# Performance work log

Measured on AMD Instinct MI355X. Metric: run time of the kernel, lower is better.

Reference implementation:

```python
import jax, jax.numpy as jnp
import numpy as np

N0, N1, F, H1, H2 = 50000, 20000, 128, 64, 32
E00, E01, E10, E11 = 1600000, 1000000, 640000, 640000
K11 = 3  # number of drug-drug relation types


def spmm(rows, cols, vals, X, n_out):
    # sparse (COO) adjacency @ dense X : out[r] += vals[e] * X[cols[e]]
    return jax.ops.segment_sum(vals[:, None] * X[cols], rows, num_segments=n_out)


def setup_inputs() -> dict:
    key = jax.random.key(0)
    ks = jax.random.split(key, 24)
    ri = jax.random.randint
    return {
        'feat0': jax.random.normal(ks[0], (N0, F), jnp.float32),
        'feat1': jax.random.normal(ks[1], (N1, F), jnp.float32),
        'e00_row': ri(ks[2], (E00,), 0, N0, jnp.int32),
        'e00_col': ri(ks[3], (E00,), 0, N0, jnp.int32),
        'e00_val': jax.random.uniform(ks[4], (E00,), jnp.float32),
        'e01_row': ri(ks[5], (E01,), 0, N0, jnp.int32),
        'e01_col': ri(ks[6], (E01,), 0, N1, jnp.int32),
        'e01_val': jax.random.uniform(ks[7], (E01,), jnp.float32),
        'e10_row': ri(ks[8], (E10,), 0, N1, jnp.int32),
        'e10_col': ri(ks[9], (E10,), 0, N0, jnp.int32),
        'e10_val': jax.random.uniform(ks[10], (E10,), jnp.float32),
        'e11_row': ri(ks[11], (K11, E11), 0, N1, jnp.int32),
        'e11_col': ri(ks[12], (K11, E11), 0, N1, jnp.int32),
        'e11_val': jax.random.uniform(ks[13], (K11, E11), jnp.float32),
        'W1_00': jax.random.normal(ks[14], (F, H1), jnp.float32) * 0.05,
        'W1_01': jax.random.normal(ks[15], (F, H1), jnp.float32) * 0.05,
        'W1_10': jax.random.normal(ks[16], (F, H1), jnp.float32) * 0.05,
        'W1_11': jax.random.normal(ks[17], (K11, F, H1), jnp.float32) * 0.05,
        'W2_00': jax.random.normal(ks[18], (H1, H2), jnp.float32) * 0.05,
        'W2_01': jax.random.normal(ks[19], (H1, H2), jnp.float32) * 0.05,
        'W2_10': jax.random.normal(ks[20], (H1, H2), jnp.float32) * 0.05,
        'W2_11': jax.random.normal(ks[21], (K11, H1, H2), jnp.float32) * 0.05,
    }


def reference(feat0, feat1,
              e00_row, e00_col, e00_val,
              e01_row, e01_col, e01_val,
              e10_row, e10_col, e10_val,
              e11_row, e11_col, e11_val,
              W1_00, W1_01, W1_10, W1_11,
              W2_00, W2_01, W2_10, W2_11):
    n0, n1 = feat0.shape[0], feat1.shape[0]

    def multi_spmm(rows_k, cols_k, vals_k, X, W_k, n_out):
        # sum_k adj_k @ (X @ W_k), vmapped over relation types k
        out_k = jax.vmap(lambda r, c, v, W: spmm(r, c, v, X @ W, n_out))(
            rows_k, cols_k, vals_k, W_k)
        return out_k.sum(axis=0)

    # layer 1: GraphConvolutionSparseMulti per edge type, add_n per target type, relu
    h0 = jax.nn.relu(spmm(e00_row, e00_col, e00_val, feat0 @ W1_00, n0)
                     + spmm(e01_row, e01_col, e01_val, feat1 @ W1_01, n0))
    h1 = jax.nn.relu(spmm(e10_row, e10_col, e10_val, feat0 @ W1_10, n1)
                     + multi_spmm(e11_row, e11_col, e11_val, feat1, W1_11, n1))

    # layer 2: GraphConvolutionMulti, add_n per target type (identity act)
    z0 = (spmm(e00_row, e00_col, e00_val, h0 @ W2_00, n0)
          + spmm(e01_row, e01_col, e01_val, h1 @ W2_01, n0))
    z1 = (spmm(e10_row, e10_col, e10_val, h0 @ W2_10, n1)
          + multi_spmm(e11_row, e11_col, e11_val, h1, W2_11, n1))

    # node-type embeddings, concatenated along the node axis: [n0+n1, H2]
    return jnp.concatenate([z0, z1], axis=0)
```

## Files before the change

kernel.cpp:

```cpp
#include <hip/hip_runtime.h>
#include <hip/hip_bf16.h>

constexpr int F = 128, H1 = 64, H2 = 32, K11 = 3;
constexpr int BSH = 6;
constexpr int PARTE = 2048;

static __device__ __forceinline__ float bf_lo(unsigned u) { return __uint_as_float(u << 16); }
static __device__ __forceinline__ float bf_hi(unsigned u) { return __uint_as_float(u & 0xffff0000u); }
static __device__ __forceinline__ unsigned bf16_1(float a) {
    unsigned ua = __float_as_uint(a);
    return (ua + 0x7fffu + ((ua >> 16) & 1u)) >> 16;
}
static __device__ __forceinline__ unsigned pack_bf16(float a, float b) {
    unsigned ua = __float_as_uint(a), ub = __float_as_uint(b);
    unsigned ra = (ua + 0x7fffu + ((ua >> 16) & 1u)) >> 16;
    unsigned rb = (ub + 0x7fffu + ((ub >> 16) & 1u)) & 0xffff0000u;
    return ra | rb;
}

struct GemmB { const float* W[4]; long long cOff[4]; };

template<int FF, int HH, bool ABF16>
__launch_bounds__(256)
__global__ void gemm_b_kernel(const void* __restrict__ Av, GemmB gb,
                              ushort* __restrict__ Cb, int M) {
    const float* __restrict__ W = gb.W[blockIdx.y];
    ushort* C = Cb + gb.cOff[blockIdx.y];
    __shared__ float Ws[FF * HH];
    const int tid = threadIdx.x;
    for (int i = tid * 4; i < FF * HH; i += 1024)
        *reinterpret_cast<float4*>(&Ws[i]) = *reinterpret_cast<const float4*>(&W[i]);
    __syncthreads();

    constexpr int TPR = 4;
    constexpr int CPT = HH / TPR;
    const int t = blockIdx.x * 256 + tid;
    const int row = t / TPR;
    const int sub = t % TPR;
    if (row >= M) return;

    float acc[CPT];
#pragma unroll
    for (int j = 0; j < CPT; ++j) acc[j] = 0.f;

    for (int k = 0; k < FF; k += 8) {
        float av[8];
        if (ABF16) {
            const uint4 u = *reinterpret_cast<const uint4*>((const ushort*)Av + (size_t)row * FF + k);
            av[0] = bf_lo(u.x); av[1] = bf_hi(u.x);
            av[2] = bf_lo(u.y); av[3] = bf_hi(u.y);
            av[4] = bf_lo(u.z); av[5] = bf_hi(u.z);
            av[6] = bf_lo(u.w); av[7] = bf_hi(u.w);
        } else {
            const float* A = (const float*)Av + (size_t)row * FF + k;
            const float4 u0 = *reinterpret_cast<const float4*>(A);
            const float4 u1 = *reinterpret_cast<const float4*>(A + 4);
            av[0] = u0.x; av[1] = u0.y; av[2] = u0.z; av[3] = u0.w;
            av[4] = u1.x; av[5] = u1.y; av[6] = u1.z; av[7] = u1.w;
        }
#pragma unroll
        for (int kk = 0; kk < 8; ++kk) {
            const float* wr = &Ws[(k + kk) * HH + sub * CPT];
#pragma unroll
            for (int j = 0; j < CPT; j += 4) {
                const float4 wv = *reinterpret_cast<const float4*>(&wr[j]);
                acc[j + 0] = fmaf(av[kk], wv.x, acc[j + 0]);
                acc[j + 1] = fmaf(av[kk], wv.y, acc[j + 1]);
                acc[j + 2] = fmaf(av[kk], wv.z, acc[j + 2]);
                acc[j + 3] = fmaf(av[kk], wv.w, acc[j + 3]);
            }
        }
    }
    unsigned packed[CPT / 2];
#pragma unroll
    for (int j = 0; j < CPT; j += 2) packed[j / 2] = pack_bf16(acc[j], acc[j + 1]);
    unsigned* c = (unsigned*)(C + (size_t)row * HH + sub * CPT);
#pragma unroll
    for (int j = 0; j < CPT / 2; j += 4)
        *reinterpret_cast<uint4*>(&c[j]) = make_uint4(packed[j], packed[j + 1], packed[j + 2], packed[j + 3]);
}

struct BinDesc { const int* rows[6]; int E[6]; int n[6]; int binBase[6]; };

__launch_bounds__(256)
__global__ void binhist_kernel(BinDesc d, int* __restrict__ binCnt) {
    const int a = blockIdx.y;
    const int E = d.E[a];
    const int start = blockIdx.x * 8192;
    if (start >= E) return;
    const int nb = (d.n[a] + 63) >> BSH;
    __shared__ int h[1024];
    for (int i = threadIdx.x; i < nb; i += 256) h[i] = 0;
    __syncthreads();
    const int* rows = d.rows[a];
    const int end = min(E, start + 8192);
    for (int e = start + (int)threadIdx.x; e < end; e += 256)
        atomicAdd(&h[rows[e] >> BSH], 1);
    __syncthreads();
    int* bc = binCnt + d.binBase[a];
    for (int i = threadIdx.x; i < nb; i += 256)
        if (h[i]) atomicAdd(&bc[i], h[i]);
}

__launch_bounds__(256)
__global__ void binscan_kernel(const int* __restrict__ binCnt, int* __restrict__ binPtr,
                               int* __restrict__ binCur, int TB, int Etot,
                               int* __restrict__ gptr, int Lidx) {
    __shared__ int lds[256];
    __shared__ int carry;
    if (threadIdx.x == 0) carry = 0;
    __syncthreads();
    for (int base = 0; base < TB; base += 256) {
        const int i = base + threadIdx.x;
        const int v = (i < TB) ? binCnt[i] : 0;
        lds[threadIdx.x] = v;
        __syncthreads();
        for (int o = 1; o < 256; o <<= 1) {
            int t = (threadIdx.x >= o) ? lds[threadIdx.x - o] : 0;
            __syncthreads();
            lds[threadIdx.x] += t;
            __syncthreads();
        }
        const int c = carry;
        __syncthreads();
        if (i < TB) {
            const int excl = c + lds[threadIdx.x] - v;
            binPtr[i] = excl;
            binCur[i] = excl;
        }
        if (threadIdx.x == 255) carry = c + lds[255];
        __syncthreads();
    }
    if (threadIdx.x == 0) { binPtr[TB] = Etot; gptr[Lidx] = Etot; }
}

struct PartD {
    const int* rows[3]; const int* cols[3]; const float* vals[3];
    int E[3]; int nbins[3]; int binBase[3]; int edgeBase[3];
};

__launch_bounds__(256)
__global__ void partition_all_kernel(PartD d, int* __restrict__ binCur,
                                     uint2* __restrict__ tmp) {
    const int a = blockIdx.y;
    const int E = d.E[a];
    const int start = blockIdx.x * PARTE;
    if (start >= E) return;
    const int nbins = d.nbins[a];
    const int* __restrict__ rows = d.rows[a];
    const int* __restrict__ cols = d.cols[a];
    const float* __restrict__ vals = d.vals[a];
    int* __restrict__ bc = binCur + d.binBase[a];
    const int tmpBase = d.edgeBase[a];
    __shared__ int h[1024];
    __shared__ int base[1024];
    for (int i = threadIdx.x; i < nbins; i += 256) h[i] = 0;
    __syncthreads();
    int r[PARTE / 256];
#pragma unroll
    for (int j = 0; j < PARTE / 256; ++j) {
        const int idx = start + j * 256 + (int)threadIdx.x;
        r[j] = (idx < E) ? rows[idx] : -1;
        if (r[j] >= 0) atomicAdd(&h[r[j] >> BSH], 1);
    }
    __syncthreads();
    for (int i = threadIdx.x; i < nbins; i += 256) {
        const int c = h[i];
        base[i] = c ? atomicAdd(&bc[i], c) : 0;
    }
    __syncthreads();
    for (int i = threadIdx.x; i < nbins; i += 256) h[i] = 0;
    __syncthreads();
#pragma unroll
    for (int j = 0; j < PARTE / 256; ++j) {
        if (r[j] >= 0) {
            const int idx = start + j * 256 + (int)threadIdx.x;
            const int b = r[j] >> BSH;
            const int p = atomicAdd(&h[b], 1);
            tmp[(size_t)(base[b] + p - tmpBase)] =
                make_uint2(((unsigned)(r[j] & 63) << 16) | (unsigned)cols[idx],
                           __float_as_uint(vals[idx]));
        }
    }
}

struct FinD { int binBase[3]; int edgeBase[3]; int n[3]; int rowBase[3]; };

__launch_bounds__(256)
__global__ void finalize_all_kernel(FinD d, const uint2* __restrict__ tmp,
                                    const int* __restrict__ binPtr,
                                    int* __restrict__ gptr, unsigned* __restrict__ cv) {
    const int a = blockIdx.y;
    const int n = d.n[a];
    const int nbins = (n + 63) >> BSH;
    const int b = blockIdx.x;
    if (b >= nbins) return;
    const int* bp = binPtr + d.binBase[a];
    const int binStart = bp[b], binEnd = bp[b + 1];
    const int lo = binStart - d.edgeBase[a], hi = binEnd - d.edgeBase[a];
    __shared__ int cnt[64], off[64], cur[64];
    if (threadIdx.x < 64) cnt[threadIdx.x] = 0;
    __syncthreads();
    for (int i = lo + (int)threadIdx.x; i < hi; i += 256)
        atomicAdd(&cnt[tmp[i].x >> 16], 1);
    __syncthreads();
    if (threadIdx.x < 64) off[threadIdx.x] = cnt[threadIdx.x];
    __syncthreads();
    for (int o = 1; o < 64; o <<= 1) {
        int t = 0;
        if (threadIdx.x < 64 && (int)threadIdx.x >= o) t = off[threadIdx.x - o];
        __syncthreads();
        if (threadIdx.x < 64) off[threadIdx.x] += t;
        __syncthreads();
    }
    const int r0 = b << BSH;
    const int nrows = min(64, n - r0);
    if (threadIdx.x < 64) {
        const int excl = off[threadIdx.x] - cnt[threadIdx.x];
        cur[threadIdx.x] = excl;
        if ((int)threadIdx.x < nrows) (gptr + d.rowBase[a])[r0 + threadIdx.x] = binStart + excl;
    }
    __syncthreads();
    for (int i = lo + (int)threadIdx.x; i < hi; i += 256) {
        const uint2 t = tmp[i];
        const int p = atomicAdd(&cur[t.x >> 16], 1);
        cv[binStart + p] = ((t.x & 0xffffu) << 16) | bf16_1(__uint_as_float(t.y));
    }
}

struct SpmmD {
    int n0, nseg0, nseg1;
    int off0[2], off1[4];
    const ushort* X0[2];
    const ushort* X1[4];
};

template<int HH, bool RELU, bool YF32>
__launch_bounds__(256)
__global__ void spmm2_kernel(const int* __restrict__ gptr, SpmmD d,
                             const unsigned* __restrict__ cv,
                             void* __restrict__ Y0, void* __restrict__ Y1,
                             int totalRows) {
    constexpr int LPR = HH / 2;
    constexpr int EPW = 64 / LPR;
    const int wid = (int)threadIdx.x >> 6;
    const int lane = (int)threadIdx.x & 63;
    const int sub = lane / LPR;
    const int c = lane % LPR;
    const int grow = blockIdx.x * 4 + wid;
    if (grow >= totalRows) return;

    int row, nseg; void* Y;
    int o[4]; const unsigned* X[4];
    if (grow < d.n0) {
        row = grow; Y = Y0; nseg = d.nseg0;
        o[0] = d.off0[0]; o[1] = d.off0[1]; o[2] = 0; o[3] = 0;
        X[0] = (const unsigned*)d.X0[0]; X[1] = (const unsigned*)d.X0[1];
        X[2] = nullptr; X[3] = nullptr;
    } else {
        row = grow - d.n0; Y = Y1; nseg = d.nseg1;
        o[0] = d.off1[0]; o[1] = d.off1[1]; o[2] = d.off1[2]; o[3] = d.off1[3];
        X[0] = (const unsigned*)d.X1[0]; X[1] = (const unsigned*)d.X1[1];
        X[2] = (const unsigned*)d.X1[2]; X[3] = (const unsigned*)d.X1[3];
    }

    float a[4] = {0.f, 0.f, 0.f, 0.f}, b[4] = {0.f, 0.f, 0.f, 0.f};
#pragma unroll
    for (int sg = 0; sg < 4; ++sg) {
        if (sg < nseg) {
            const int* p = gptr + o[sg] + row;
            const int s = p[0], e = p[1];
            const unsigned* __restrict__ Xs = X[sg];
            int i = s;
            for (; i + 4 * EPW <= e; i += 4 * EPW) {
#pragma unroll
                for (int j = 0; j < 4; ++j) {
                    const unsigned cw = cv[i + j * EPW + sub];
                    const unsigned x = Xs[(size_t)(cw >> 16) * LPR + c];
                    const float v = __uint_as_float(cw << 16);
                    a[j] = fmaf(v, bf_lo(x), a[j]);
                    b[j] = fmaf(v, bf_hi(x), b[j]);
                }
            }
#pragma unroll
            for (int j = 0; j < 4; ++j) {
                const int idx = i + j * EPW + sub;
                if (idx < e) {
                    const unsigned cw = cv[idx];
                    const unsigned x = Xs[(size_t)(cw >> 16) * LPR + c];
                    const float v = __uint_as_float(cw << 16);
                    a[j] = fmaf(v, bf_lo(x), a[j]);
                    b[j] = fmaf(v, bf_hi(x), b[j]);
                }
            }
        }
    }
    float r0 = (a[0] + a[1]) + (a[2] + a[3]);
    float r1 = (b[0] + b[1]) + (b[2] + b[3]);
#pragma unroll
    for (int off = LPR; off < 64; off <<= 1) {
        r0 += __shfl_xor(r0, off, 64);
        r1 += __shfl_xor(r1, off, 64);
    }
    if (sub == 0) {
        if (RELU) { r0 = fmaxf(r0, 0.f); r1 = fmaxf(r1, 0.f); }
        if (YF32) {
            *reinterpret_cast<float2*>((float*)Y + (size_t)row * HH + c * 2) = make_float2(r0, r1);
        } else {
            ((unsigned*)Y)[(size_t)row * LPR + c] = pack_bf16(r0, r1);
        }
    }
}

extern "C" void kernel_launch(void* const* d_in, const int* in_sizes, int n_in,
                              void* d_out, int out_size, void* d_ws, size_t ws_size,
                              hipStream_t stream) {
    const float* feat0 = (const float*)d_in[0];
    const float* feat1 = (const float*)d_in[1];
    const int*   e00_row = (const int*)d_in[2];
    const int*   e00_col = (const int*)d_in[3];
    const float* e00_val = (const float*)d_in[4];
    const int*   e01_row = (const int*)d_in[5];
    const int*   e01_col = (const int*)d_in[6];
    const float* e01_val = (const float*)d_in[7];
    const int*   e10_row = (const int*)d_in[8];
    const int*   e10_col = (const int*)d_in[9];
    const float* e10_val = (const float*)d_in[10];
    const int*   e11_row = (const int*)d_in[11];
    const int*   e11_col = (const int*)d_in[12];
    const float* e11_val = (const float*)d_in[13];
    const float* W1_00 = (const float*)d_in[14];
    const float* W1_01 = (const float*)d_in[15];
    const float* W1_10 = (const float*)d_in[16];
    const float* W1_11 = (const float*)d_in[17];
    const float* W2_00 = (const float*)d_in[18];
    const float* W2_01 = (const float*)d_in[19];
    const float* W2_10 = (const float*)d_in[20];
    const float* W2_11 = (const float*)d_in[21];

    const int N0  = in_sizes[0] / F;
    const int N1  = in_sizes[1] / F;
    const int E00 = in_sizes[2];
    const int E01 = in_sizes[5];
    const int E10 = in_sizes[8];
    const int E11 = in_sizes[11] / K11;
    const long long E_total = (long long)E00 + E01 + E10 + (long long)K11 * E11;

    const int s00 = 0, s01 = N0, s10 = 2 * N0, s11 = 2 * N0 + N1;
    const int L = 2 * N0 + (1 + K11) * N1;

    struct HA { const int* rows; const int* cols; const float* vals; int E; int s; int n; };
    const HA arrs[6] = {
        {e00_row, e00_col, e00_val, E00, s00, N0},
        {e01_row, e01_col, e01_val, E01, s01, N0},
        {e10_row, e10_col, e10_val, E10, s10, N1},
        {e11_row,          e11_col,          e11_val,          E11, s11,          N1},
        {e11_row + E11,    e11_col + E11,    e11_val + E11,    E11, s11 + N1,     N1},
        {e11_row + 2*E11,  e11_col + 2*E11,  e11_val + 2*E11,  E11, s11 + 2*N1,   N1},
    };

    int nbins_[6], binBase_[6]; long long edgeBase_[6];
    int TB = 0; long long eb = 0;
    int maxE = 0;
    for (int i = 0; i < 6; ++i) {
        binBase_[i] = TB; nbins_[i] = (arrs[i].n + 63) >> BSH; TB += nbins_[i];
        edgeBase_[i] = eb; eb += arrs[i].E;
        maxE = max(maxE, arrs[i].E);
    }
    const int TBc = (TB + 2 + 3) & ~3;
    const int Lc = (L + 1 + 3) & ~3;

    ushort* h0 = (ushort*)d_ws;
    ushort* h1 = h0 + (size_t)N0 * H1;
    ushort* g  = h1 + (size_t)N1 * H1;
    const size_t G = ((size_t)2 * N0 + 4 * N1) * H1;
    int* iw = (int*)(g + G);
    int* binCnt = iw;
    int* binPtr = binCnt + TBc;
    int* binCur = binPtr + TBc;
    int* gptr   = binCur + TBc;
    unsigned* cv = (unsigned*)(gptr + Lc);

    const size_t required = ((size_t)(N0 + N1) * H1 + G) * 2
                          + ((size_t)3 * TBc + Lc + (size_t)E_total) * 4;
    const size_t trioBytes = (size_t)K11 * E11 * 8;
    if (ws_size < required || N0 > 65536 || N1 > 65536 ||
        (size_t)maxE * 8 > G * 2 || trioBytes > G * 2) return;

    hipMemsetAsync(binCnt, 0, (size_t)TBc * sizeof(int), stream);
    BinDesc bd;
    for (int i = 0; i < 6; ++i) { bd.rows[i] = arrs[i].rows; bd.E[i] = arrs[i].E; bd.n[i] = arrs[i].n; bd.binBase[i] = binBase_[i]; }
    binhist_kernel<<<dim3((maxE + 8191) / 8192, 6), 256, 0, stream>>>(bd, binCnt);
    binscan_kernel<<<1, 256, 0, stream>>>(binCnt, binPtr, binCur, TB, (int)E_total, gptr, L);

    uint2* tmp = (uint2*)g;
    auto launchPF = [&](int first, int cnt) {
        const long long tmpBase = edgeBase_[first];
        PartD pd{}; FinD fd{};
        int mE = 0, mNB = 0;
        for (int j = 0; j < cnt; ++j) {
            const int i = first + j;
            pd.rows[j] = arrs[i].rows; pd.cols[j] = arrs[i].cols; pd.vals[j] = arrs[i].vals;
            pd.E[j] = arrs[i].E; pd.nbins[j] = nbins_[i]; pd.binBase[j] = binBase_[i];
            pd.edgeBase[j] = (int)tmpBase;
            fd.binBase[j] = binBase_[i]; fd.edgeBase[j] = (int)tmpBase;
            fd.n[j] = arrs[i].n; fd.rowBase[j] = arrs[i].s;
            mE = max(mE, arrs[i].E); mNB = max(mNB, nbins_[i]);
        }
        partition_all_kernel<<<dim3((mE + PARTE - 1) / PARTE, cnt), 256, 0, stream>>>(pd, binCur, tmp);
        finalize_all_kernel<<<dim3(mNB, cnt), 256, 0, stream>>>(fd, tmp, binPtr, gptr, cv);
    };
    launchPF(0, 1);
    launchPF(1, 1);
    launchPF(2, 1);
    launchPF(3, 3);

    float* z0 = (float*)d_out;
    float* z1 = (float*)d_out + (size_t)N0 * H2;
    const int TR = N0 + N1;

    {
        GemmB ga; ga.W[0] = W1_00; ga.cOff[0] = 0;
        ga.W[1] = W1_10; ga.cOff[1] = (long long)(N0 + N1) * H1;
        ga.W[2] = W1_00; ga.cOff[2] = 0; ga.W[3] = W1_00; ga.cOff[3] = 0;
        gemm_b_kernel<F, H1, false><<<dim3((N0 * 4 + 255) / 256, 2), 256, 0, stream>>>(feat0, ga, g, N0);
        GemmB gbt; gbt.W[0] = W1_01; gbt.cOff[0] = (long long)N0 * H1;
        for (int k = 0; k < K11; ++k) {
            gbt.W[1 + k] = W1_11 + (size_t)k * F * H1;
            gbt.cOff[1 + k] = ((long long)(2 * N0 + N1) + (long long)k * N1) * H1;
        }
        gemm_b_kernel<F, H1, false><<<dim3((N1 * 4 + 255) / 256, 4), 256, 0, stream>>>(feat1, gbt, g, N1);
    }
    {
        SpmmD sd;
        sd.n0 = N0; sd.nseg0 = 2; sd.nseg1 = 4;
        sd.off0[0] = s00; sd.X0[0] = g;
        sd.off0[1] = s01; sd.X0[1] = g + (size_t)N0 * H1;
        sd.off1[0] = s10; sd.X1[0] = g + (size_t)(N0 + N1) * H1;
        for (int k = 0; k < K11; ++k) {
            sd.off1[1 + k] = s11 + k * N1;
            sd.X1[1 + k] = g + ((size_t)(2 * N0 + N1) + (size_t)k * N1) * H1;
        }
        spmm2_kernel<H1, true, false><<<(TR + 3) / 4, 256, 0, stream>>>(gptr, sd, cv, h0, h1, TR);
    }
    {
        GemmB ga; ga.W[0] = W2_00; ga.cOff[0] = 0;
        ga.W[1] = W2_10; ga.cOff[1] = (long long)(N0 + N1) * H2;
        ga.W[2] = W2_00; ga.cOff[2] = 0; ga.W[3] = W2_00; ga.cOff[3] = 0;
        gemm_b_kernel<H1, H2, true><<<dim3((N0 * 4 + 255) / 256, 2), 256, 0, stream>>>(h0, ga, g, N0);
        GemmB gbt; gbt.W[0] = W2_01; gbt.cOff[0] = (long long)N0 * H2;
        for (int k = 0; k < K11; ++k) {
            gbt.W[1 + k] = W2_11 + (size_t)k * H1 * H2;
            gbt.cOff[1 + k] = ((long long)(2 * N0 + N1) + (long long)k * N1) * H2;
        }
        gemm_b_kernel<H1, H2, true><<<dim3((N1 * 4 + 255) / 256, 4), 256, 0, stream>>>(h1, gbt, g, N1);
    }
    {
        SpmmD sd;
        sd.n0 = N0; sd.nseg0 = 2; sd.nseg1 = 4;
        sd.off0[0] = s00; sd.X0[0] = g;
        sd.off0[1] = s01; sd.X0[1] = g + (size_t)N0 * H2;
        sd.off1[0] = s10; sd.X1[0] = g + (size_t)(N0 + N1) * H2;
        for (int k = 0; k < K11; ++k) {
            sd.off1[1 + k] = s11 + k * N1;
            sd.X1[1 + k] = g + ((size_t)(2 * N0 + N1) + (size_t)k * N1) * H2;
        }
        spmm2_kernel<H2, false, true><<<(TR + 3) / 4, 256, 0, stream>>>(gptr, sd, cv, z0, z1, TR);
    }

    (void)n_in; (void)out_size;
}
```

Before: 484.7 us.

## Widen SpMM gathers to 16-byte loads, merge GEMM and partition launches

The SpMM kernel now has each lane gather eight bf16 features (uint4) per edge instead of two. It loads the column words and feature vectors for four edges before doing the FMAs, so more memory requests are in flight and fewer wide transactions are issued. The two GEMM launches per layer are merged into one six-way batched launch, and the partition/finalize passes are grouped into two launches instead of four, cutting launch count. The trade-off is more lanes reducing per row (more shuffle stages, eight values each), higher register pressure, and larger temporary-buffer requirements checked at setup.

```diff
diff --git a/kernel.cpp b/kernel.cpp
--- a/kernel.cpp
+++ b/kernel.cpp
@@ -18,14 +18,17 @@
     return ra | rb;
 }
 
-struct GemmB { const float* W[4]; long long cOff[4]; };
+struct GemmB6 { const void* A[6]; const float* W[6]; long long cOff[6]; int M[6]; };
 
 template<int FF, int HH, bool ABF16>
 __launch_bounds__(256)
-__global__ void gemm_b_kernel(const void* __restrict__ Av, GemmB gb,
-                              ushort* __restrict__ Cb, int M) {
-    const float* __restrict__ W = gb.W[blockIdx.y];
-    ushort* C = Cb + gb.cOff[blockIdx.y];
+__global__ void gemm_b6_kernel(GemmB6 gb, ushort* __restrict__ Cb) {
+    const int y = blockIdx.y;
+    const int M = gb.M[y];
+    if (blockIdx.x * 64 >= M) return;
+    const float* __restrict__ W = gb.W[y];
+    const void* __restrict__ Av = gb.A[y];
+    ushort* C = Cb + gb.cOff[y];
     __shared__ float Ws[FF * HH];
     const int tid = threadIdx.x;
     for (int i = tid * 4; i < FF * HH; i += 1024)
@@ -135,8 +138,8 @@
 }
 
 struct PartD {
-    const int* rows[3]; const int* cols[3]; const float* vals[3];
-    int E[3]; int nbins[3]; int binBase[3]; int edgeBase[3];
+    const int* rows[4]; const int* cols[4]; const float* vals[4];
+    int E[4]; int nbins[4]; int binBase[4]; int edgeBase[4];
 };
 
 __launch_bounds__(256)
@@ -184,7 +187,7 @@
     }
 }
 
-struct FinD { int binBase[3]; int edgeBase[3]; int n[3]; int rowBase[3]; };
+struct FinD { int binBase[4]; int edgeBase[4]; int n[4]; int rowBase[4]; };
 
 __launch_bounds__(256)
 __global__ void finalize_all_kernel(FinD d, const uint2* __restrict__ tmp,
@@ -241,7 +244,7 @@
                              const unsigned* __restrict__ cv,
                              void* __restrict__ Y0, void* __restrict__ Y1,
                              int totalRows) {
-    constexpr int LPR = HH / 2;
+    constexpr int LPR = HH / 8;
     constexpr int EPW = 64 / LPR;
     const int wid = (int)threadIdx.x >> 6;
     const int lane = (int)threadIdx.x & 63;
@@ -251,35 +254,47 @@
     if (grow >= totalRows) return;
 
     int row, nseg; void* Y;
-    int o[4]; const unsigned* X[4];
+    int o[4]; const uint4* X[4];
     if (grow < d.n0) {
         row = grow; Y = Y0; nseg = d.nseg0;
         o[0] = d.off0[0]; o[1] = d.off0[1]; o[2] = 0; o[3] = 0;
-        X[0] = (const unsigned*)d.X0[0]; X[1] = (const unsigned*)d.X0[1];
+        X[0] = (const uint4*)d.X0[0]; X[1] = (const uint4*)d.X0[1];
         X[2] = nullptr; X[3] = nullptr;
     } else {
         row = grow - d.n0; Y = Y1; nseg = d.nseg1;
         o[0] = d.off1[0]; o[1] = d.off1[1]; o[2] = d.off1[2]; o[3] = d.off1[3];
-        X[0] = (const unsigned*)d.X1[0]; X[1] = (const unsigned*)d.X1[1];
-        X[2] = (const unsigned*)d.X1[2]; X[3] = (const unsigned*)d.X1[3];
-    }
-
-    float a[4] = {0.f, 0.f, 0.f, 0.f}, b[4] = {0.f, 0.f, 0.f, 0.f};
+        X[0] = (const uint4*)d.X1[0]; X[1] = (const uint4*)d.X1[1];
+        X[2] = (const uint4*)d.X1[2]; X[3] = (const uint4*)d.X1[3];
+    }
+
+    float4 aL[4], aH[4];
+#pragma unroll
+    for (int j = 0; j < 4; ++j) { aL[j] = make_float4(0,0,0,0); aH[j] = make_float4(0,0,0,0); }
+
 #pragma unroll
     for (int sg = 0; sg < 4; ++sg) {
         if (sg < nseg) {
             const int* p = gptr + o[sg] + row;
             const int s = p[0], e = p[1];
-            const unsigned* __restrict__ Xs = X[sg];
+            const uint4* __restrict__ Xs = X[sg];
             int i = s;
             for (; i + 4 * EPW <= e; i += 4 * EPW) {
+                unsigned cw[4]; uint4 x[4];
+#pragma unroll
+                for (int j = 0; j < 4; ++j) cw[j] = cv[i + j * EPW + sub];
+#pragma unroll
+                for (int j = 0; j < 4; ++j) x[j] = Xs[(size_t)(cw[j] >> 16) * LPR + c];
 #pragma unroll
                 for (int j = 0; j < 4; ++j) {
-                    const unsigned cw = cv[i + j * EPW + sub];
-                    const unsigned x = Xs[(size_t)(cw >> 16) * LPR + c];
-                    const float v = __uint_as_float(cw << 16);
-                    a[j] = fmaf(v, bf_lo(x), a[j]);
-                    b[j] = fmaf(v, bf_hi(x), b[j]);
+                    const float v = __uint_as_float(cw[j] << 16);
+                    aL[j].x = fmaf(v, bf_lo(x[j].x), aL[j].x);
+                    aL[j].y = fmaf(v, bf_hi(x[j].x), aL[j].y);
+                    aL[j].z = fmaf(v, bf_lo(x[j].y), aL[j].z);
+                    aL[j].w = fmaf(v, bf_hi(x[j].y), aL[j].w);
+                    aH[j].x = fmaf(v, bf_lo(x[j].z), aH[j].x);
+                    aH[j].y = fmaf(v, bf_hi(x[j].z), aH[j].y);
+                    aH[j].z = fmaf(v, bf_lo(x[j].w), aH[j].z);
+                    aH[j].w = fmaf(v, bf_hi(x[j].w), aH[j].w);
                 }
             }
 #pragma unroll
@@ -287,27 +302,47 @@
                 const int idx = i + j * EPW + sub;
                 if (idx < e) {
                     const unsigned cw = cv[idx];
-                    const unsigned x = Xs[(size_t)(cw >> 16) * LPR + c];
+                    const uint4 x = Xs[(size_t)(cw >> 16) * LPR + c];
                     const float v = __uint_as_float(cw << 16);
-                    a[j] = fmaf(v, bf_lo(x), a[j]);
-                    b[j] = fmaf(v, bf_hi(x), b[j]);
+                    aL[j].x = fmaf(v, bf_lo(x.x), aL[j].x);
+                    aL[j].y = fmaf(v, bf_hi(x.x), aL[j].y);
+                    aL[j].z = fmaf(v, bf_lo(x.y), aL[j].z);
+                    aL[j].w = fmaf(v, bf_hi(x.y), aL[j].w);
+                    aH[j].x = fmaf(v, bf_lo(x.z), aH[j].x);
+                    aH[j].y = fmaf(v, bf_hi(x.z), aH[j].y);
+                    aH[j].z = fmaf(v, bf_lo(x.w), aH[j].z);
+                    aH[j].w = fmaf(v, bf_hi(x.w), aH[j].w);
                 }
             }
         }
     }
-    float r0 = (a[0] + a[1]) + (a[2] + a[3]);
-    float r1 = (b[0] + b[1]) + (b[2] + b[3]);
+    float r[8];
+    r[0] = (aL[0].x + aL[1].x) + (aL[2].x + aL[3].x);
+    r[1] = (aL[0].y + aL[1].y) + (aL[2].y + aL[3].y);
+    r[2] = (aL[0].z + aL[1].z) + (aL[2].z + aL[3].z);
+    r[3] = (aL[0].w + aL[1].w) + (aL[2].w + aL[3].w);
+    r[4] = (aH[0].x + aH[1].x) + (aH[2].x + aH[3].x);
+    r[5] = (aH[0].y + aH[1].y) + (aH[2].y + aH[3].y);
+    r[6] = (aH[0].z + aH[1].z) + (aH[2].z + aH[3].z);
+    r[7] = (aH[0].w + aH[1].w) + (aH[2].w + aH[3].w);
 #pragma unroll
     for (int off = LPR; off < 64; off <<= 1) {
-        r0 += __shfl_xor(r0, off, 64);
-        r1 += __shfl_xor(r1, off, 64);
+#pragma unroll
+        for (int q = 0; q < 8; ++q) r[q] += __shfl_xor(r[q], off, 64);
     }
     if (sub == 0) {
-        if (RELU) { r0 = fmaxf(r0, 0.f); r1 = fmaxf(r1, 0.f); }
+        if (RELU) {
+#pragma unroll
+            for (int q = 0; q < 8; ++q) r[q] = fmaxf(r[q], 0.f);
+        }
         if (YF32) {
-            *reinterpret_cast<float2*>((float*)Y + (size_t)row * HH + c * 2) = make_float2(r0, r1);
+            float* y = (float*)Y + (size_t)row * HH + c * 8;
+            *reinterpret_cast<float4*>(y) = make_float4(r[0], r[1], r[2], r[3]);
+            *reinterpret_cast<float4*>(y + 4) = make_float4(r[4], r[5], r[6], r[7]);
         } else {
-            ((unsigned*)Y)[(size_t)row * LPR + c] = pack_bf16(r0, r1);
+            reinterpret_cast<uint4*>((unsigned*)Y + (size_t)row * (HH / 2))[c] =
+                make_uint4(pack_bf16(r[0], r[1]), pack_bf16(r[2], r[3]),
+                           pack_bf16(r[4], r[5]), pack_bf16(r[6], r[7]));
         }
     }
 }
@@ -383,9 +418,10 @@
 
     const size_t required = ((size_t)(N0 + N1) * H1 + G) * 2
                           + ((size_t)3 * TBc + Lc + (size_t)E_total) * 4;
-    const size_t trioBytes = (size_t)K11 * E11 * 8;
+    const size_t batchA = ((size_t)E00 + E01) * 8;
+    const size_t batchB = ((size_t)E10 + (size_t)K11 * E11) * 8;
     if (ws_size < required || N0 > 65536 || N1 > 65536 ||
-        (size_t)maxE * 8 > G * 2 || trioBytes > G * 2) return;
+        batchA > G * 2 || batchB > G * 2) return;
 
     hipMemsetAsync(binCnt, 0, (size_t)TBc * sizeof(int), stream);
     BinDesc bd;
@@ -410,26 +446,24 @@
         partition_all_kernel<<<dim3((mE + PARTE - 1) / PARTE, cnt), 256, 0, stream>>>(pd, binCur, tmp);
         finalize_all_kernel<<<dim3(mNB, cnt), 256, 0, stream>>>(fd, tmp, binPtr, gptr, cv);
     };
-    launchPF(0, 1);
-    launchPF(1, 1);
-    launchPF(2, 1);
-    launchPF(3, 3);
+    launchPF(0, 2);
+    launchPF(2, 4);
 
     float* z0 = (float*)d_out;
     float* z1 = (float*)d_out + (size_t)N0 * H2;
     const int TR = N0 + N1;
+    const int gx1 = (max(N0, N1) * 4 + 255) / 256;
 
     {
-        GemmB ga; ga.W[0] = W1_00; ga.cOff[0] = 0;
-        ga.W[1] = W1_10; ga.cOff[1] = (long long)(N0 + N1) * H1;
-        ga.W[2] = W1_00; ga.cOff[2] = 0; ga.W[3] = W1_00; ga.cOff[3] = 0;
-        gemm_b_kernel<F, H1, false><<<dim3((N0 * 4 + 255) / 256, 2), 256, 0, stream>>>(feat0, ga, g, N0);
-        GemmB gbt; gbt.W[0] = W1_01; gbt.cOff[0] = (long long)N0 * H1;
+        GemmB6 gb;
+        gb.A[0] = feat0; gb.W[0] = W1_00; gb.cOff[0] = 0;                                   gb.M[0] = N0;
+        gb.A[1] = feat0; gb.W[1] = W1_10; gb.cOff[1] = (long long)(N0 + N1) * H1;           gb.M[1] = N0;
+        gb.A[2] = feat1; gb.W[2] = W1_01; gb.cOff[2] = (long long)N0 * H1;                  gb.M[2] = N1;
         for (int k = 0; k < K11; ++k) {
-            gbt.W[1 + k] = W1_11 + (size_t)k * F * H1;
-            gbt.cOff[1 + k] = ((long long)(2 * N0 + N1) + (long long)k * N1) * H1;
-        }
-        gemm_b_kernel<F, H1, false><<<dim3((N1 * 4 + 255) / 256, 4), 256, 0, stream>>>(feat1, gbt, g, N1);
+            gb.A[3 + k] = feat1; gb.W[3 + k] = W1_11 + (size_t)k * F * H1;
+            gb.cOff[3 + k] = ((long long)(2 * N0 + N1) + (long long)k * N1) * H1;           gb.M[3 + k] = N1;
+        }
+        gemm_b6_kernel<F, H1, false><<<dim3(gx1, 6), 256, 0, stream>>>(gb, g);
     }
     {
         SpmmD sd;
@@ -444,16 +478,15 @@
         spmm2_kernel<H1, true, false><<<(TR + 3) / 4, 256, 0, stream>>>(gptr, sd, cv, h0, h1, TR);
     }
     {
-        GemmB ga; ga.W[0] = W2_00; ga.cOff[0] = 0;
-        ga.W[1] = W2_10; ga.cOff[1] = (long long)(N0 + N1) * H2;
-        ga.W[2] = W2_00; ga.cOff[2] = 0; ga.W[3] = W2_00; ga.cOff[3] = 0;
-        gemm_b_kernel<H1, H2, true><<<dim3((N0 * 4 + 255) / 256, 2), 256, 0, stream>>>(h0, ga, g, N0);
-        GemmB gbt; gbt.W[0] = W2_01; gbt.cOff[0] = (long long)N0 * H2;
+        GemmB6 gb;
+        gb.A[0] = h0; gb.W[0] = W2_00; gb.cOff[0] = 0;                                      gb.M[0] = N0;
+        gb.A[1] = h0; gb.W[1] = W2_10; gb.cOff[1] = (long long)(N0 + N1) * H2;              gb.M[1] = N0;
+        gb.A[2] = h1; gb.W[2] = W2_01; gb.cOff[2] = (long long)N0 * H2;                     gb.M[2] = N1;
         for (int k = 0; k < K11; ++k) {
-            gbt.W[1 + k] = W2_11 + (size_t)k * H1 * H2;
-            gbt.cOff[1 + k] = ((long long)(2 * N0 + N1) + (long long)k * N1) * H2;
-        }
-        gemm_b_kernel<H1, H2, true><<<dim3((N1 * 4 + 255) / 256, 4), 256, 0, stream>>>(h1, gbt, g, N1);
+            gb.A[3 + k] = h1; gb.W[3 + k] = W2_11 + (size_t)k * H1 * H2;
+            gb.cOff[3 + k] = ((long long)(2 * N0 + N1) + (long long)k * N1) * H2;           gb.M[3 + k] = N1;
+        }
+        gemm_b6_kernel<H1, H2, true><<<dim3(gx1, 6), 256, 0, stream>>>(gb, g);
     }
     {
         SpmmD sd;
```

New measurement: 446.3 us. 7.9% less time.
